# Kernel optimization log

Hardware: AMD Instinct MI355X
Metric: run time of the kernel (lower is better)

Reference implementation:

```python
import jax, jax.numpy as jnp
import numpy as np

K = 512          # num_embeddings
D = 8            # latent_dim
DECAY = 0.99     # ema_decay
EPS = 1e-5


def setup_inputs() -> dict:
    key = jax.random.key(0)
    k1, k2 = jax.random.split(key)
    z = jax.random.normal(k1, (64, D, 64, 64), dtype=jnp.float32)
    # codebook initialized uniform(-1/K, 1/K) as in the torch module
    codebook = jax.random.uniform(k2, (K, D), dtype=jnp.float32,
                                  minval=-1.0 / K, maxval=1.0 / K)
    ema_cluster_size = jnp.zeros((K,), dtype=jnp.float32)
    ema_w = jnp.zeros((K, D), dtype=jnp.float32)
    return {"z": z, "codebook": codebook,
            "ema_cluster_size": ema_cluster_size, "ema_w": ema_w}


def reference(z, codebook, ema_cluster_size, ema_w):
    B, C, H, W = z.shape
    # (B, HW, C) flattened latents, matching z.view(B,C,-1).permute(0,2,1)
    flat = z.reshape(B, C, H * W).transpose(0, 2, 1)

    # cdist p=2: ||z||^2 - 2 z.e + ||e||^2, then sqrt (argmin unaffected,
    # but we keep the sqrt for faithfulness to torch.cdist)
    z_sq = jnp.sum(flat * flat, axis=-1, keepdims=True)        # (B, N, 1)
    e_sq = jnp.sum(codebook * codebook, axis=-1)               # (K,)
    dots = jnp.einsum('bnd,kd->bnk', flat, codebook)           # (B, N, K)
    distances = jnp.sqrt(jnp.maximum(z_sq - 2.0 * dots + e_sq, 0.0))

    indices = jnp.argmin(distances, axis=-1)                   # (B, N) int

    # embedding gather with the OLD codebook (as in the torch forward)
    z_q = codebook[indices]                                    # (B, N, D)
    z_q = z_q.transpose(0, 2, 1).reshape(B, C, H, W)

    commitment_loss = jnp.mean((jax.lax.stop_gradient(z_q) - z) ** 2)
    loss = commitment_loss  # use_ema=True branch

    # ---- EMA in-place codebook update (buffers) ----
    idx_flat = indices.reshape(-1)                             # (B*N,)
    inp_flat = flat.reshape(-1, C)                             # (B*N, D)
    counts = jax.ops.segment_sum(jnp.ones_like(idx_flat, dtype=z.dtype),
                                 idx_flat, num_segments=K)     # (K,)
    sums = jax.ops.segment_sum(inp_flat, idx_flat, num_segments=K)  # (K, D)

    new_cs = ema_cluster_size * DECAY + counts * (1.0 - DECAY)
    new_w = ema_w * DECAY + sums * (1.0 - DECAY)
    n = jnp.sum(new_cs)
    cs_smoothed = (new_cs + EPS) / (n + K * EPS) * n
    new_codebook = new_w / cs_smoothed[:, None]

    return z_q, loss, new_codebook, cs_smoothed, new_w
```

## Files before the change

kernel.cpp:

```cpp
#include <hip/hip_runtime.h>

constexpr int Kc   = 512;
constexpr int Dc   = 8;
constexpr int HWc  = 4096;
constexpr int CHWc = Dc * HWc;
constexpr int Mc   = 64 * HWc;
constexpr int TOTALc = Mc * Dc;

constexpr int REP      = 8;
constexpr int RSTRIDE  = 4616;
constexpr int ACC_FLOATS = REP * RSTRIDE;

typedef float v2f  __attribute__((ext_vector_type(2)));
typedef unsigned long long ull;
typedef ull  u64x4 __attribute__((ext_vector_type(4)));

__global__ __launch_bounds__(256) void vq_prep(const float* __restrict__ cb,
                                               float* __restrict__ ws) {
    const int tid = blockIdx.x * 256 + threadIdx.x;
    float4* w4 = (float4*)ws;
    for (int i = tid; i < ACC_FLOATS / 4; i += gridDim.x * 256)
        w4[i] = float4{0.f, 0.f, 0.f, 0.f};
    if (blockIdx.x == 0) {
        for (int k = threadIdx.x; k < Kc; k += 256) {
            float s = 0.f;
#pragma unroll
            for (int c = 0; c < Dc; ++c) {
                const float e = cb[k * Dc + c];
                s = fmaf(e, e, s);
            }
            ws[ACC_FLOATS + k] = s;
        }
    }
}

__global__ __launch_bounds__(512, 8) void vq_main(const float* __restrict__ z,
                                                  const float* __restrict__ cb,
                                                  const float* __restrict__ esq,
                                                  float* __restrict__ ws,
                                                  float* __restrict__ zq) {
    __shared__ float s_mn[8][256];
    __shared__ int   s_im[8][256];
    __shared__ float s_counts[Kc];
    __shared__ float s_sums[Kc * Dc];
    __shared__ float s_loss;

    const int t = threadIdx.x;
    for (int i = t; i < Kc; i += 512) s_counts[i] = 0.f;
    for (int i = t; i < Kc * Dc; i += 512) s_sums[i] = 0.f;
    if (t == 0) s_loss = 0.f;

    const int l = t & 63;
    const int g  = __builtin_amdgcn_readfirstlane(t >> 6);
    const int k0 = g << 6;

    const int base = blockIdx.x * 256;
    const int b  = base >> 12;
    const int n0 = (base & (HWc - 1)) + l;
    const float* zb = z + b * CHWc + n0;

    v2f zzA[Dc], zzB[Dc];
#pragma unroll
    for (int c = 0; c < Dc; ++c) {
        zzA[c] = v2f{-2.0f * zb[c * HWc],       -2.0f * zb[c * HWc + 64]};
        zzB[c] = v2f{-2.0f * zb[c * HWc + 128], -2.0f * zb[c * HWc + 192]};
    }
    asm("" : "+v"(zzA[0]), "+v"(zzA[1]), "+v"(zzA[2]), "+v"(zzA[3]),
             "+v"(zzA[4]), "+v"(zzA[5]), "+v"(zzA[6]), "+v"(zzA[7]),
             "+v"(zzB[0]), "+v"(zzB[1]), "+v"(zzB[2]), "+v"(zzB[3]),
             "+v"(zzB[4]), "+v"(zzB[5]), "+v"(zzB[6]), "+v"(zzB[7]));

    const float* cbg = cb + (k0 << 3);
    const float* eqg = esq + k0;

    float mn0 = 3.4e38f, mn1 = 3.4e38f, mn2 = 3.4e38f, mn3 = 3.4e38f;
    int   i0 = k0, i1 = k0, i2 = k0, i3 = k0;

#define SLOAD(R0, R1, EV, ROFF, EOFF)                                  \
    asm volatile("s_load_dwordx8 %0, %3, %5\n\t"                       \
                 "s_load_dwordx8 %1, %3, %6\n\t"                       \
                 "s_load_dwordx2 %2, %4, %7"                           \
                 : "=s"(R0), "=s"(R1), "=s"(EV)                        \
                 : "s"(cbg), "s"(eqg),                                 \
                   "s"(ROFF), "s"((ROFF) + 32), "s"(EOFF))

#define PKSTEP(Q, P0, P1)                                              \
    asm volatile(                                                      \
        "v_pk_fma_f32 %0, %2, %4, %0 op_sel_hi:[1,0,1]\n\t"            \
        "v_pk_fma_f32 %1, %3, %4, %1 op_sel_hi:[1,0,1]\n\t"            \
        "v_pk_fma_f32 %0, %5, %4, %0 op_sel:[0,1,0]\n\t"               \
        "v_pk_fma_f32 %1, %6, %4, %1 op_sel:[0,1,0]"                   \
        : "+v"(aA), "+v"(aB)                                           \
        : "v"(zzA[P0]), "v"(zzB[P0]), "s"(Q), "v"(zzA[P1]), "v"(zzB[P1]))

#define CODE1(ROW, EVF, KK)                                            \
    {                                                                  \
        const float ev_ = (EVF);                                       \
        const v2f vev2 = {ev_, ev_};                                   \
        v2f aA, aB;                                                    \
        asm volatile(                                                  \
            "v_pk_fma_f32 %0, %2, %4, %5 op_sel_hi:[1,0,1]\n\t"        \
            "v_pk_fma_f32 %1, %3, %4, %5 op_sel_hi:[1,0,1]\n\t"        \
            "v_pk_fma_f32 %0, %6, %4, %0 op_sel:[0,1,0]\n\t"           \
            "v_pk_fma_f32 %1, %7, %4, %1 op_sel:[0,1,0]"               \
            : "=&v"(aA), "=&v"(aB)                                     \
            : "v"(zzA[0]), "v"(zzB[0]), "s"((ROW).x), "v"(vev2),       \
              "v"(zzA[1]), "v"(zzB[1]));                               \
        PKSTEP((ROW).y, 2, 3);                                         \
        PKSTEP((ROW).z, 4, 5);                                         \
        PKSTEP((ROW).w, 6, 7);                                         \
        const float a0 = aA.x, a1 = aA.y, a2 = aB.x, a3 = aB.y;        \
        bool c_;                                                       \
        c_ = a0 < mn0; mn0 = c_ ? a0 : mn0; i0 = c_ ? (KK) : i0;       \
        c_ = a1 < mn1; mn1 = c_ ? a1 : mn1; i1 = c_ ? (KK) : i1;       \
        c_ = a2 < mn2; mn2 = c_ ? a2 : mn2; i2 = c_ ? (KK) : i2;       \
        c_ = a3 < mn3; mn3 = c_ ? a3 : mn3; i3 = c_ ? (KK) : i3;       \
    }

#define PIPE_STEP(C0, C1, CEV, N0, N1, NEV, KK)                        \
    asm volatile("s_waitcnt lgkmcnt(0)");                              \
    __builtin_amdgcn_sched_barrier(0);                                 \
    {                                                                  \
        const int ro_ = ro > 1984 ? 1984 : ro;                         \
        const int eo_ = eo > 248  ? 248  : eo;                         \
        SLOAD(N0, N1, NEV, ro_, eo_);                                  \
        ro += 64; eo += 8;                                             \
    }                                                                  \
    __builtin_amdgcn_sched_barrier(0);                                 \
    CODE1(C0, (CEV)[0], KK);                                           \
    CODE1(C1, (CEV)[1], (KK) + 1);

    u64x4 A0, A1, B0, B1;
    v2f   Aev, Bev;
    int ro = 0, eo = 0;
    SLOAD(A0, A1, Aev, 0, 0);
    ro = 64; eo = 8;
    int kk = k0;
#pragma unroll 1
    for (int hs = 0; hs < 16; ++hs) {
        PIPE_STEP(A0, A1, Aev, B0, B1, Bev, kk);
        PIPE_STEP(B0, B1, Bev, A0, A1, Aev, kk + 2);
        kk += 4;
    }

#undef PIPE_STEP
#undef CODE1
#undef PKSTEP
#undef SLOAD

    s_mn[g][l]       = mn0;  s_im[g][l]       = i0;
    s_mn[g][l +  64] = mn1;  s_im[g][l +  64] = i1;
    s_mn[g][l + 128] = mn2;  s_im[g][l + 128] = i2;
    s_mn[g][l + 192] = mn3;  s_im[g][l + 192] = i3;
    __syncthreads();

    if (t < 256) {
        const int v = t;
        float mn = s_mn[0][v];
        int   im = s_im[0][v];
#pragma unroll
        for (int gg = 1; gg < 8; ++gg) {
            const float m2 = s_mn[gg][v];
            const int   j2 = s_im[gg][v];
            const bool  c2 = m2 < mn;
            mn = c2 ? m2 : mn;
            im = c2 ? j2 : im;
        }

        const float4* cb4 = (const float4*)cb;
        const float4 qa = cb4[im * 2], qb = cb4[im * 2 + 1];
        const float q[Dc] = {qa.x, qa.y, qa.z, qa.w, qb.x, qb.y, qb.z, qb.w};

        const int nv = (base & (HWc - 1)) + v;
        const float* zv = z + b * CHWc + nv;
        float* zqv = zq + b * CHWc + nv;
        float lsum = 0.f;
        float zr[Dc];
#pragma unroll
        for (int c = 0; c < Dc; ++c) {
            zr[c] = zv[c * HWc];
            zqv[c * HWc] = q[c];
            const float d = q[c] - zr[c];
            lsum = fmaf(d, d, lsum);
        }

        unsafeAtomicAdd(&s_counts[im], 1.0f);
#pragma unroll
        for (int c = 0; c < Dc; ++c)
            unsafeAtomicAdd(&s_sums[im * Dc + c], zr[c]);
        unsafeAtomicAdd(&s_loss, lsum);
    }
    __syncthreads();

    float* acc = ws + (blockIdx.x & (REP - 1)) * RSTRIDE;
    for (int i = t; i < Kc; i += 512) {
        const float val = s_counts[i];
        if (val != 0.f) unsafeAtomicAdd(&acc[i], val);
    }
    for (int i = t; i < Kc * Dc; i += 512) {
        const float val = s_sums[i];
        if (val != 0.f) unsafeAtomicAdd(&acc[512 + i], val);
    }
    if (t == 0) unsafeAtomicAdd(&acc[4608], s_loss);
}

__global__ __launch_bounds__(512) void vq_final(const float* __restrict__ ws,
                                                const float* __restrict__ ema_cs,
                                                const float* __restrict__ ema_w,
                                                float* __restrict__ out) {
    constexpr float DEC  = 0.99f;
    constexpr float OMD  = (float)(1.0 - 0.99);
    constexpr float EPSf = 1e-5f;
    constexpr float KEPS = (float)(512 * 1e-5);
    __shared__ float red[512];
    __shared__ float s_cs[512];

    const int t = threadIdx.x;
    float cnt = 0.f;
#pragma unroll
    for (int r = 0; r < REP; ++r) cnt += ws[r * RSTRIDE + t];
    const float ncs = ema_cs[t] * DEC + cnt * OMD;
    red[t] = ncs;
    __syncthreads();
    for (int s = 256; s > 0; s >>= 1) {
        if (t < s) red[t] += red[t + s];
        __syncthreads();
    }
    const float n  = red[0];
    const float cs = (ncs + EPSf) / (n + KEPS) * n;
    s_cs[t] = cs;

    float* out_loss = out + TOTALc;
    float* out_cb   = out + TOTALc + 1;
    float* out_cs   = out_cb + Kc * Dc;
    float* out_nw   = out_cs + Kc;

    __syncthreads();

    const int blk = blockIdx.x;
    if (blk == 0) {
        out_cs[t] = cs;
        if (t == 0) {
            float ls = 0.f;
#pragma unroll
            for (int r = 0; r < REP; ++r) ls += ws[r * RSTRIDE + 4608];
            out_loss[0] = ls * (1.0f / 2097152.0f);
        }
    } else {
        const int e = (blk - 1) * 512 + t;
        float sm = 0.f;
#pragma unroll
        for (int r = 0; r < REP; ++r) sm += ws[r * RSTRIDE + 512 + e];
        const float nw = ema_w[e] * DEC + sm * OMD;
        out_nw[e] = nw;
        out_cb[e] = nw / s_cs[e >> 3];
    }
}

extern "C" void kernel_launch(void* const* d_in, const int* in_sizes, int n_in,
                              void* d_out, int out_size, void* d_ws, size_t ws_size,
                              hipStream_t stream) {
    const float* z      = (const float*)d_in[0];
    const float* cb     = (const float*)d_in[1];
    const float* ema_cs = (const float*)d_in[2];
    const float* ema_w  = (const float*)d_in[3];
    float* out = (float*)d_out;
    float* ws  = (float*)d_ws;

    vq_prep<<<32, 256, 0, stream>>>(cb, ws);
    vq_main<<<Mc / 256, 512, 0, stream>>>(z, cb, ws + ACC_FLOATS, ws, out);
    vq_final<<<9, 512, 0, stream>>>(ws, ema_cs, ema_w, out);
}
```

Before: 108.6 us.

## Give each thread full codebook scan over two points, dropping cross-wave argmin merge

Rather than splitting the 512 codes across 8 waves and merging partial argmins through shared memory, each thread now scans all 512 codes for 2 points, so each block handles 1024 points and the grid is 4x smaller. This removes the shared-memory argmin reduction and the second read of z, since z is recovered from the pre-scaled registers. The loss is reduced with a wavefront shuffle before the shared atomic. The trade-off is far fewer blocks (256) and a serial chain of 512 codes per thread, which cuts latency hiding and shrinks the grid to roughly one block per CU.

```diff
diff --git a/kernel.cpp b/kernel.cpp
--- a/kernel.cpp
+++ b/kernel.cpp
@@ -39,8 +39,6 @@
                                                   const float* __restrict__ esq,
                                                   float* __restrict__ ws,
                                                   float* __restrict__ zq) {
-    __shared__ float s_mn[8][256];
-    __shared__ int   s_im[8][256];
     __shared__ float s_counts[Kc];
     __shared__ float s_sums[Kc * Dc];
     __shared__ float s_loss;
@@ -50,79 +48,63 @@
     for (int i = t; i < Kc * Dc; i += 512) s_sums[i] = 0.f;
     if (t == 0) s_loss = 0.f;
 
-    const int l = t & 63;
-    const int g  = __builtin_amdgcn_readfirstlane(t >> 6);
-    const int k0 = g << 6;
-
-    const int base = blockIdx.x * 256;
+    const int base = blockIdx.x * 1024;
     const int b  = base >> 12;
-    const int n0 = (base & (HWc - 1)) + l;
+    const int n0 = (base & (HWc - 1)) + t;
     const float* zb = z + b * CHWc + n0;
 
-    v2f zzA[Dc], zzB[Dc];
-#pragma unroll
-    for (int c = 0; c < Dc; ++c) {
-        zzA[c] = v2f{-2.0f * zb[c * HWc],       -2.0f * zb[c * HWc + 64]};
-        zzB[c] = v2f{-2.0f * zb[c * HWc + 128], -2.0f * zb[c * HWc + 192]};
-    }
-    asm("" : "+v"(zzA[0]), "+v"(zzA[1]), "+v"(zzA[2]), "+v"(zzA[3]),
-             "+v"(zzA[4]), "+v"(zzA[5]), "+v"(zzA[6]), "+v"(zzA[7]),
-             "+v"(zzB[0]), "+v"(zzB[1]), "+v"(zzB[2]), "+v"(zzB[3]),
-             "+v"(zzB[4]), "+v"(zzB[5]), "+v"(zzB[6]), "+v"(zzB[7]));
-
-    const float* cbg = cb + (k0 << 3);
-    const float* eqg = esq + k0;
-
-    float mn0 = 3.4e38f, mn1 = 3.4e38f, mn2 = 3.4e38f, mn3 = 3.4e38f;
-    int   i0 = k0, i1 = k0, i2 = k0, i3 = k0;
+    v2f zz[Dc];
+#pragma unroll
+    for (int c = 0; c < Dc; ++c)
+        zz[c] = v2f{-2.0f * zb[c * HWc], -2.0f * zb[c * HWc + 512]};
+    asm("" : "+v"(zz[0]), "+v"(zz[1]), "+v"(zz[2]), "+v"(zz[3]),
+             "+v"(zz[4]), "+v"(zz[5]), "+v"(zz[6]), "+v"(zz[7]));
+
+    float mn0 = 3.4e38f, mn1 = 3.4e38f;
+    int   i0 = 0, i1 = 0;
 
 #define SLOAD(R0, R1, EV, ROFF, EOFF)                                  \
     asm volatile("s_load_dwordx8 %0, %3, %5\n\t"                       \
                  "s_load_dwordx8 %1, %3, %6\n\t"                       \
                  "s_load_dwordx2 %2, %4, %7"                           \
                  : "=s"(R0), "=s"(R1), "=s"(EV)                        \
-                 : "s"(cbg), "s"(eqg),                                 \
+                 : "s"(cb), "s"(esq),                                  \
                    "s"(ROFF), "s"((ROFF) + 32), "s"(EOFF))
-
-#define PKSTEP(Q, P0, P1)                                              \
-    asm volatile(                                                      \
-        "v_pk_fma_f32 %0, %2, %4, %0 op_sel_hi:[1,0,1]\n\t"            \
-        "v_pk_fma_f32 %1, %3, %4, %1 op_sel_hi:[1,0,1]\n\t"            \
-        "v_pk_fma_f32 %0, %5, %4, %0 op_sel:[0,1,0]\n\t"               \
-        "v_pk_fma_f32 %1, %6, %4, %1 op_sel:[0,1,0]"                   \
-        : "+v"(aA), "+v"(aB)                                           \
-        : "v"(zzA[P0]), "v"(zzB[P0]), "s"(Q), "v"(zzA[P1]), "v"(zzB[P1]))
 
 #define CODE1(ROW, EVF, KK)                                            \
     {                                                                  \
         const float ev_ = (EVF);                                       \
         const v2f vev2 = {ev_, ev_};                                   \
-        v2f aA, aB;                                                    \
-        asm volatile(                                                  \
-            "v_pk_fma_f32 %0, %2, %4, %5 op_sel_hi:[1,0,1]\n\t"        \
-            "v_pk_fma_f32 %1, %3, %4, %5 op_sel_hi:[1,0,1]\n\t"        \
-            "v_pk_fma_f32 %0, %6, %4, %0 op_sel:[0,1,0]\n\t"           \
-            "v_pk_fma_f32 %1, %7, %4, %1 op_sel:[0,1,0]"               \
-            : "=&v"(aA), "=&v"(aB)                                     \
-            : "v"(zzA[0]), "v"(zzB[0]), "s"((ROW).x), "v"(vev2),       \
-              "v"(zzA[1]), "v"(zzB[1]));                               \
-        PKSTEP((ROW).y, 2, 3);                                         \
-        PKSTEP((ROW).z, 4, 5);                                         \
-        PKSTEP((ROW).w, 6, 7);                                         \
-        const float a0 = aA.x, a1 = aA.y, a2 = aB.x, a3 = aB.y;        \
+        v2f aA;                                                        \
+        asm volatile(                                                  \
+            "v_pk_fma_f32 %0, %1, %2, %3 op_sel_hi:[1,0,1]\n\t"        \
+            "v_pk_fma_f32 %0, %4, %2, %0 op_sel:[0,1,0]"               \
+            : "=&v"(aA)                                                \
+            : "v"(zz[0]), "s"((ROW).x), "v"(vev2), "v"(zz[1]));        \
+        asm volatile(                                                  \
+            "v_pk_fma_f32 %0, %1, %2, %0 op_sel_hi:[1,0,1]\n\t"        \
+            "v_pk_fma_f32 %0, %3, %2, %0 op_sel:[0,1,0]"               \
+            : "+v"(aA) : "v"(zz[2]), "s"((ROW).y), "v"(zz[3]));        \
+        asm volatile(                                                  \
+            "v_pk_fma_f32 %0, %1, %2, %0 op_sel_hi:[1,0,1]\n\t"        \
+            "v_pk_fma_f32 %0, %3, %2, %0 op_sel:[0,1,0]"               \
+            : "+v"(aA) : "v"(zz[4]), "s"((ROW).z), "v"(zz[5]));        \
+        asm volatile(                                                  \
+            "v_pk_fma_f32 %0, %1, %2, %0 op_sel_hi:[1,0,1]\n\t"        \
+            "v_pk_fma_f32 %0, %3, %2, %0 op_sel:[0,1,0]"               \
+            : "+v"(aA) : "v"(zz[6]), "s"((ROW).w), "v"(zz[7]));        \
+        const float a0 = aA.x, a1 = aA.y;                              \
         bool c_;                                                       \
         c_ = a0 < mn0; mn0 = c_ ? a0 : mn0; i0 = c_ ? (KK) : i0;       \
         c_ = a1 < mn1; mn1 = c_ ? a1 : mn1; i1 = c_ ? (KK) : i1;       \
-        c_ = a2 < mn2; mn2 = c_ ? a2 : mn2; i2 = c_ ? (KK) : i2;       \
-        c_ = a3 < mn3; mn3 = c_ ? a3 : mn3; i3 = c_ ? (KK) : i3;       \
     }
 
 #define PIPE_STEP(C0, C1, CEV, N0, N1, NEV, KK)                        \
     asm volatile("s_waitcnt lgkmcnt(0)");                              \
     __builtin_amdgcn_sched_barrier(0);                                 \
     {                                                                  \
-        const int ro_ = ro > 1984 ? 1984 : ro;                         \
-        const int eo_ = eo > 248  ? 248  : eo;                         \
+        const int ro_ = ro > 16320 ? 16320 : ro;                       \
+        const int eo_ = eo > 2040  ? 2040  : eo;                       \
         SLOAD(N0, N1, NEV, ro_, eo_);                                  \
         ro += 64; eo += 8;                                             \
     }                                                                  \
@@ -135,9 +117,9 @@
     int ro = 0, eo = 0;
     SLOAD(A0, A1, Aev, 0, 0);
     ro = 64; eo = 8;
-    int kk = k0;
+    int kk = 0;
 #pragma unroll 1
-    for (int hs = 0; hs < 16; ++hs) {
+    for (int hs = 0; hs < 128; ++hs) {
         PIPE_STEP(A0, A1, Aev, B0, B1, Bev, kk);
         PIPE_STEP(B0, B1, Bev, A0, A1, Aev, kk + 2);
         kk += 4;
@@ -145,51 +127,50 @@
 
 #undef PIPE_STEP
 #undef CODE1
-#undef PKSTEP
 #undef SLOAD
 
-    s_mn[g][l]       = mn0;  s_im[g][l]       = i0;
-    s_mn[g][l +  64] = mn1;  s_im[g][l +  64] = i1;
-    s_mn[g][l + 128] = mn2;  s_im[g][l + 128] = i2;
-    s_mn[g][l + 192] = mn3;  s_im[g][l + 192] = i3;
-    __syncthreads();
-
-    if (t < 256) {
-        const int v = t;
-        float mn = s_mn[0][v];
-        int   im = s_im[0][v];
-#pragma unroll
-        for (int gg = 1; gg < 8; ++gg) {
-            const float m2 = s_mn[gg][v];
-            const int   j2 = s_im[gg][v];
-            const bool  c2 = m2 < mn;
-            mn = c2 ? m2 : mn;
-            im = c2 ? j2 : im;
-        }
-
-        const float4* cb4 = (const float4*)cb;
-        const float4 qa = cb4[im * 2], qb = cb4[im * 2 + 1];
+    __syncthreads();
+
+    const float4* cb4 = (const float4*)cb;
+    float lsum = 0.f;
+    {
+        const float4 qa = cb4[i0 * 2], qb = cb4[i0 * 2 + 1];
         const float q[Dc] = {qa.x, qa.y, qa.z, qa.w, qb.x, qb.y, qb.z, qb.w};
-
-        const int nv = (base & (HWc - 1)) + v;
-        const float* zv = z + b * CHWc + nv;
-        float* zqv = zq + b * CHWc + nv;
-        float lsum = 0.f;
+        float* zqv = zq + b * CHWc + n0;
         float zr[Dc];
 #pragma unroll
         for (int c = 0; c < Dc; ++c) {
-            zr[c] = zv[c * HWc];
+            zr[c] = -0.5f * zz[c].x;
             zqv[c * HWc] = q[c];
             const float d = q[c] - zr[c];
             lsum = fmaf(d, d, lsum);
         }
-
-        unsafeAtomicAdd(&s_counts[im], 1.0f);
+        unsafeAtomicAdd(&s_counts[i0], 1.0f);
 #pragma unroll
         for (int c = 0; c < Dc; ++c)
-            unsafeAtomicAdd(&s_sums[im * Dc + c], zr[c]);
-        unsafeAtomicAdd(&s_loss, lsum);
-    }
+            unsafeAtomicAdd(&s_sums[i0 * Dc + c], zr[c]);
+    }
+    {
+        const float4 qa = cb4[i1 * 2], qb = cb4[i1 * 2 + 1];
+        const float q[Dc] = {qa.x, qa.y, qa.z, qa.w, qb.x, qb.y, qb.z, qb.w};
+        float* zqv = zq + b * CHWc + n0 + 512;
+        float zr[Dc];
+#pragma unroll
+        for (int c = 0; c < Dc; ++c) {
+            zr[c] = -0.5f * zz[c].y;
+            zqv[c * HWc] = q[c];
+            const float d = q[c] - zr[c];
+            lsum = fmaf(d, d, lsum);
+        }
+        unsafeAtomicAdd(&s_counts[i1], 1.0f);
+#pragma unroll
+        for (int c = 0; c < Dc; ++c)
+            unsafeAtomicAdd(&s_sums[i1 * Dc + c], zr[c]);
+    }
+#pragma unroll
+    for (int s = 32; s > 0; s >>= 1)
+        lsum += __shfl_down(lsum, s);
+    if ((t & 63) == 0) unsafeAtomicAdd(&s_loss, lsum);
     __syncthreads();
 
     float* acc = ws + (blockIdx.x & (REP - 1)) * RSTRIDE;
@@ -268,6 +249,6 @@
     float* ws  = (float*)d_ws;
 
     vq_prep<<<32, 256, 0, stream>>>(cb, ws);
-    vq_main<<<Mc / 256, 512, 0, stream>>>(z, cb, ws + ACC_FLOATS, ws, out);
+    vq_main<<<Mc / 1024, 512, 0, stream>>>(z, cb, ws + ACC_FLOATS, ws, out);
     vq_final<<<9, 512, 0, stream>>>(ws, ema_cs, ema_w, out);
 }
```

After: 143.8 us. 1.32x slower.

## Process 512 points per block with 8 points per lane for codebook reuse

Applied to the files above, without the earlier changes.

Each block now handles 512 latent vectors instead of 256, so every lane holds eight points and each scalar-loaded codebook row is reused across twice as many FMAs. This halves the grid size, along with the per-block shared-memory zeroing and the global atomic flushes of the histogram and sums. The loss is reduced with a wavefront shuffle before a single shared atomic per wave, rather than one atomic per thread. The cost is higher register use, with launch bounds lowered to allow 4 blocks per CU instead of 8, which may reduce occupancy and latency hiding.

```diff
diff --git a/kernel.cpp b/kernel.cpp
--- a/kernel.cpp
+++ b/kernel.cpp
@@ -34,13 +34,13 @@
     }
 }
 
-__global__ __launch_bounds__(512, 8) void vq_main(const float* __restrict__ z,
+__global__ __launch_bounds__(512, 4) void vq_main(const float* __restrict__ z,
                                                   const float* __restrict__ cb,
                                                   const float* __restrict__ esq,
                                                   float* __restrict__ ws,
                                                   float* __restrict__ zq) {
-    __shared__ float s_mn[8][256];
-    __shared__ int   s_im[8][256];
+    __shared__ float s_mn[8][512];
+    __shared__ int   s_im[8][512];
     __shared__ float s_counts[Kc];
     __shared__ float s_sums[Kc * Dc];
     __shared__ float s_loss;
@@ -54,27 +54,35 @@
     const int g  = __builtin_amdgcn_readfirstlane(t >> 6);
     const int k0 = g << 6;
 
-    const int base = blockIdx.x * 256;
+    const int base = blockIdx.x * 512;
     const int b  = base >> 12;
     const int n0 = (base & (HWc - 1)) + l;
     const float* zb = z + b * CHWc + n0;
 
-    v2f zzA[Dc], zzB[Dc];
+    v2f zz0[Dc], zz1[Dc], zz2[Dc], zz3[Dc];
 #pragma unroll
     for (int c = 0; c < Dc; ++c) {
-        zzA[c] = v2f{-2.0f * zb[c * HWc],       -2.0f * zb[c * HWc + 64]};
-        zzB[c] = v2f{-2.0f * zb[c * HWc + 128], -2.0f * zb[c * HWc + 192]};
-    }
-    asm("" : "+v"(zzA[0]), "+v"(zzA[1]), "+v"(zzA[2]), "+v"(zzA[3]),
-             "+v"(zzA[4]), "+v"(zzA[5]), "+v"(zzA[6]), "+v"(zzA[7]),
-             "+v"(zzB[0]), "+v"(zzB[1]), "+v"(zzB[2]), "+v"(zzB[3]),
-             "+v"(zzB[4]), "+v"(zzB[5]), "+v"(zzB[6]), "+v"(zzB[7]));
+        zz0[c] = v2f{-2.0f * zb[c * HWc],       -2.0f * zb[c * HWc +  64]};
+        zz1[c] = v2f{-2.0f * zb[c * HWc + 128], -2.0f * zb[c * HWc + 192]};
+        zz2[c] = v2f{-2.0f * zb[c * HWc + 256], -2.0f * zb[c * HWc + 320]};
+        zz3[c] = v2f{-2.0f * zb[c * HWc + 384], -2.0f * zb[c * HWc + 448]};
+    }
+    asm("" : "+v"(zz0[0]), "+v"(zz0[1]), "+v"(zz0[2]), "+v"(zz0[3]),
+             "+v"(zz0[4]), "+v"(zz0[5]), "+v"(zz0[6]), "+v"(zz0[7]));
+    asm("" : "+v"(zz1[0]), "+v"(zz1[1]), "+v"(zz1[2]), "+v"(zz1[3]),
+             "+v"(zz1[4]), "+v"(zz1[5]), "+v"(zz1[6]), "+v"(zz1[7]));
+    asm("" : "+v"(zz2[0]), "+v"(zz2[1]), "+v"(zz2[2]), "+v"(zz2[3]),
+             "+v"(zz2[4]), "+v"(zz2[5]), "+v"(zz2[6]), "+v"(zz2[7]));
+    asm("" : "+v"(zz3[0]), "+v"(zz3[1]), "+v"(zz3[2]), "+v"(zz3[3]),
+             "+v"(zz3[4]), "+v"(zz3[5]), "+v"(zz3[6]), "+v"(zz3[7]));
 
     const float* cbg = cb + (k0 << 3);
     const float* eqg = esq + k0;
 
     float mn0 = 3.4e38f, mn1 = 3.4e38f, mn2 = 3.4e38f, mn3 = 3.4e38f;
+    float mn4 = 3.4e38f, mn5 = 3.4e38f, mn6 = 3.4e38f, mn7 = 3.4e38f;
     int   i0 = k0, i1 = k0, i2 = k0, i3 = k0;
+    int   i4 = k0, i5 = k0, i6 = k0, i7 = k0;
 
 #define SLOAD(R0, R1, EV, ROFF, EOFF)                                  \
     asm volatile("s_load_dwordx8 %0, %3, %5\n\t"                       \
@@ -84,37 +92,51 @@
                  : "s"(cbg), "s"(eqg),                                 \
                    "s"(ROFF), "s"((ROFF) + 32), "s"(EOFF))
 
-#define PKSTEP(Q, P0, P1)                                              \
+#define PK8(Q, C0, C1)                                                 \
     asm volatile(                                                      \
-        "v_pk_fma_f32 %0, %2, %4, %0 op_sel_hi:[1,0,1]\n\t"            \
-        "v_pk_fma_f32 %1, %3, %4, %1 op_sel_hi:[1,0,1]\n\t"            \
-        "v_pk_fma_f32 %0, %5, %4, %0 op_sel:[0,1,0]\n\t"               \
-        "v_pk_fma_f32 %1, %6, %4, %1 op_sel:[0,1,0]"                   \
-        : "+v"(aA), "+v"(aB)                                           \
-        : "v"(zzA[P0]), "v"(zzB[P0]), "s"(Q), "v"(zzA[P1]), "v"(zzB[P1]))
+        "v_pk_fma_f32 %0, %4, %12, %0 op_sel_hi:[1,0,1]\n\t"           \
+        "v_pk_fma_f32 %1, %5, %12, %1 op_sel_hi:[1,0,1]\n\t"           \
+        "v_pk_fma_f32 %2, %6, %12, %2 op_sel_hi:[1,0,1]\n\t"           \
+        "v_pk_fma_f32 %3, %7, %12, %3 op_sel_hi:[1,0,1]\n\t"           \
+        "v_pk_fma_f32 %0, %8, %12, %0 op_sel:[0,1,0]\n\t"              \
+        "v_pk_fma_f32 %1, %9, %12, %1 op_sel:[0,1,0]\n\t"              \
+        "v_pk_fma_f32 %2, %10, %12, %2 op_sel:[0,1,0]\n\t"             \
+        "v_pk_fma_f32 %3, %11, %12, %3 op_sel:[0,1,0]"                 \
+        : "+v"(aA), "+v"(aB), "+v"(aC), "+v"(aD)                       \
+        : "v"(zz0[C0]), "v"(zz1[C0]), "v"(zz2[C0]), "v"(zz3[C0]),      \
+          "v"(zz0[C1]), "v"(zz1[C1]), "v"(zz2[C1]), "v"(zz3[C1]),      \
+          "s"(Q))
 
 #define CODE1(ROW, EVF, KK)                                            \
     {                                                                  \
         const float ev_ = (EVF);                                       \
         const v2f vev2 = {ev_, ev_};                                   \
-        v2f aA, aB;                                                    \
+        v2f aA, aB, aC, aD;                                            \
         asm volatile(                                                  \
-            "v_pk_fma_f32 %0, %2, %4, %5 op_sel_hi:[1,0,1]\n\t"        \
-            "v_pk_fma_f32 %1, %3, %4, %5 op_sel_hi:[1,0,1]\n\t"        \
-            "v_pk_fma_f32 %0, %6, %4, %0 op_sel:[0,1,0]\n\t"           \
-            "v_pk_fma_f32 %1, %7, %4, %1 op_sel:[0,1,0]"               \
-            : "=&v"(aA), "=&v"(aB)                                     \
-            : "v"(zzA[0]), "v"(zzB[0]), "s"((ROW).x), "v"(vev2),       \
-              "v"(zzA[1]), "v"(zzB[1]));                               \
-        PKSTEP((ROW).y, 2, 3);                                         \
-        PKSTEP((ROW).z, 4, 5);                                         \
-        PKSTEP((ROW).w, 6, 7);                                         \
-        const float a0 = aA.x, a1 = aA.y, a2 = aB.x, a3 = aB.y;        \
+            "v_pk_fma_f32 %0, %4, %8, %9 op_sel_hi:[1,0,1]\n\t"        \
+            "v_pk_fma_f32 %1, %5, %8, %9 op_sel_hi:[1,0,1]\n\t"        \
+            "v_pk_fma_f32 %2, %6, %8, %9 op_sel_hi:[1,0,1]\n\t"        \
+            "v_pk_fma_f32 %3, %7, %8, %9 op_sel_hi:[1,0,1]\n\t"        \
+            "v_pk_fma_f32 %0, %10, %8, %0 op_sel:[0,1,0]\n\t"          \
+            "v_pk_fma_f32 %1, %11, %8, %1 op_sel:[0,1,0]\n\t"          \
+            "v_pk_fma_f32 %2, %12, %8, %2 op_sel:[0,1,0]\n\t"          \
+            "v_pk_fma_f32 %3, %13, %8, %3 op_sel:[0,1,0]"              \
+            : "=&v"(aA), "=&v"(aB), "=&v"(aC), "=&v"(aD)               \
+            : "v"(zz0[0]), "v"(zz1[0]), "v"(zz2[0]), "v"(zz3[0]),      \
+              "s"((ROW).x), "v"(vev2),                                 \
+              "v"(zz0[1]), "v"(zz1[1]), "v"(zz2[1]), "v"(zz3[1]));     \
+        PK8((ROW).y, 2, 3);                                            \
+        PK8((ROW).z, 4, 5);                                            \
+        PK8((ROW).w, 6, 7);                                            \
         bool c_;                                                       \
-        c_ = a0 < mn0; mn0 = c_ ? a0 : mn0; i0 = c_ ? (KK) : i0;       \
-        c_ = a1 < mn1; mn1 = c_ ? a1 : mn1; i1 = c_ ? (KK) : i1;       \
-        c_ = a2 < mn2; mn2 = c_ ? a2 : mn2; i2 = c_ ? (KK) : i2;       \
-        c_ = a3 < mn3; mn3 = c_ ? a3 : mn3; i3 = c_ ? (KK) : i3;       \
+        c_ = aA.x < mn0; i0 = c_ ? (KK) : i0; mn0 = c_ ? aA.x : mn0;   \
+        c_ = aA.y < mn1; i1 = c_ ? (KK) : i1; mn1 = c_ ? aA.y : mn1;   \
+        c_ = aB.x < mn2; i2 = c_ ? (KK) : i2; mn2 = c_ ? aB.x : mn2;   \
+        c_ = aB.y < mn3; i3 = c_ ? (KK) : i3; mn3 = c_ ? aB.y : mn3;   \
+        c_ = aC.x < mn4; i4 = c_ ? (KK) : i4; mn4 = c_ ? aC.x : mn4;   \
+        c_ = aC.y < mn5; i5 = c_ ? (KK) : i5; mn5 = c_ ? aC.y : mn5;   \
+        c_ = aD.x < mn6; i6 = c_ ? (KK) : i6; mn6 = c_ ? aD.x : mn6;   \
+        c_ = aD.y < mn7; i7 = c_ ? (KK) : i7; mn7 = c_ ? aD.y : mn7;   \
     }
 
 #define PIPE_STEP(C0, C1, CEV, N0, N1, NEV, KK)                        \
@@ -145,16 +167,20 @@
 
 #undef PIPE_STEP
 #undef CODE1
-#undef PKSTEP
+#undef PK8
 #undef SLOAD
 
     s_mn[g][l]       = mn0;  s_im[g][l]       = i0;
     s_mn[g][l +  64] = mn1;  s_im[g][l +  64] = i1;
     s_mn[g][l + 128] = mn2;  s_im[g][l + 128] = i2;
     s_mn[g][l + 192] = mn3;  s_im[g][l + 192] = i3;
+    s_mn[g][l + 256] = mn4;  s_im[g][l + 256] = i4;
+    s_mn[g][l + 320] = mn5;  s_im[g][l + 320] = i5;
+    s_mn[g][l + 384] = mn6;  s_im[g][l + 384] = i6;
+    s_mn[g][l + 448] = mn7;  s_im[g][l + 448] = i7;
     __syncthreads();
 
-    if (t < 256) {
+    {
         const int v = t;
         float mn = s_mn[0][v];
         int   im = s_im[0][v];
@@ -188,7 +214,11 @@
 #pragma unroll
         for (int c = 0; c < Dc; ++c)
             unsafeAtomicAdd(&s_sums[im * Dc + c], zr[c]);
-        unsafeAtomicAdd(&s_loss, lsum);
+
+#pragma unroll
+        for (int s = 32; s > 0; s >>= 1)
+            lsum += __shfl_down(lsum, s);
+        if ((t & 63) == 0) unsafeAtomicAdd(&s_loss, lsum);
     }
     __syncthreads();
 
@@ -268,6 +298,6 @@
     float* ws  = (float*)d_ws;
 
     vq_prep<<<32, 256, 0, stream>>>(cb, ws);
-    vq_main<<<Mc / 256, 512, 0, stream>>>(z, cb, ws + ACC_FLOATS, ws, out);
+    vq_main<<<Mc / 512, 512, 0, stream>>>(z, cb, ws + ACC_FLOATS, ws, out);
     vq_final<<<9, 512, 0, stream>>>(ws, ema_cs, ema_w, out);
 }
```

After: 110.2 us. Within noise of the previous version (+1.4%).
